# Optimization experiments

Measured on AMD Instinct MI355X. Metric: run time of the kernel, lower is better.

Reference implementation:

```python
import jax, jax.numpy as jnp
import numpy as np
from jax import lax
from jax.scipy.special import logsumexp

B, T, L = 64, 256, 16          # batch, max words per sent, max chars per word
VC, DC, CH = 100, 50, 100      # char vocab, char emb dim, char cnn hidden
VW, DW = 50000, 300            # word vocab, word emb dim
VF, DF = 20, 20                # feature vocab, feature emb dim
H = 256                        # lstm hidden per direction (word_hidden_dim=512)
LAB = 50                       # label alphabet size
N = LAB + 2                    # +START, +STOP tags (NCRF++-style CRF)
START, STOP = N - 2, N - 1
IN = CH + DW + DF              # lstm input dim = 420


def setup_inputs():
    key = jax.random.key(0)
    k = jax.random.split(key, 16)
    p = 0.1
    # pack_padded_sequence requires lengths sorted descending; max length = T
    lens = jnp.sort(jax.random.randint(k[0], (B,), T // 2, T + 1))[::-1].at[0].set(T)
    mask = jnp.arange(T)[None, :] < lens[:, None]
    return dict(
        batch_word=jax.random.randint(k[1], (B, T), 0, VW),
        batch_features=jax.random.randint(k[2], (B, 1), 0, VF),
        batch_wordlen=lens,
        batch_char=jax.random.randint(k[3], (B * T, L), 0, VC),
        batch_charlen=jnp.full((B * T,), L, dtype=jnp.int32),
        batch_charrecover=jnp.arange(B * T),
        mask=mask,
        batch_label=jax.random.randint(k[4], (B, T), 0, LAB),
        char_emb=jax.random.normal(k[5], (VC, DC)) * p,
        conv_w=jax.random.normal(k[6], (CH, DC, 3)) * p,
        conv_b=jnp.zeros((CH,)),
        word_emb=jax.random.normal(k[7], (VW, DW)) * p,
        feat_emb=jax.random.normal(k[8], (VF, DF)) * p,
        w_ih_f=jax.random.normal(k[9], (4 * H, IN)) * p,
        w_hh_f=jax.random.normal(k[10], (4 * H, H)) * p,
        b_f=jnp.zeros((4 * H,)),
        w_ih_b=jax.random.normal(k[11], (4 * H, IN)) * p,
        w_hh_b=jax.random.normal(k[12], (4 * H, H)) * p,
        b_b=jnp.zeros((4 * H,)),
        proj_w=jax.random.normal(k[13], (N, 2 * H)) * p,
        proj_b=jnp.zeros((N,)),
        transitions=(jax.random.normal(k[14], (N, N)) * p)
            .at[:, START].set(-1e4).at[STOP, :].set(-1e4),
    )


def _lstm_dir(x_tb, m_tb, w_ih, w_hh, b, reverse):
    # x_tb: (T,B,IN), m_tb: (T,B,1) float; masked state update == packed-seq LSTM
    xs = jnp.einsum('tbi,gi->tbg', x_tb, w_ih) + b  # precomputed input proj
    def step(carry, inp):
        h, c = carry
        xt, mt = inp
        g = xt + h @ w_hh.T
        i, f, gg, o = jnp.split(g, 4, axis=-1)  # torch gate order i,f,g,o
        c_new = jax.nn.sigmoid(f) * c + jax.nn.sigmoid(i) * jnp.tanh(gg)
        h_new = jax.nn.sigmoid(o) * jnp.tanh(c_new)
        h = mt * h_new + (1 - mt) * h
        c = mt * c_new + (1 - mt) * c
        return (h, c), h
    init = (jnp.zeros((x_tb.shape[1], H), x_tb.dtype),
            jnp.zeros((x_tb.shape[1], H), x_tb.dtype))
    _, hs = lax.scan(step, init, (xs, m_tb), reverse=reverse)
    return hs  # (T,B,H)


def _emissions(batch_word, batch_features, batch_char, batch_charrecover, mask,
               char_emb, conv_w, conv_b, word_emb, feat_emb,
               w_ih_f, w_hh_f, b_f, w_ih_b, w_hh_b, b_b, proj_w, proj_b):
    maskf = mask.astype(jnp.float32)
    # char CNN (dropout = identity at eval time)
    ce = char_emb[batch_char].transpose(0, 2, 1)                     # (BT,DC,L)
    cc = lax.conv_general_dilated(ce, conv_w, (1,), [(1, 1)],
                                  dimension_numbers=('NCH', 'OIH', 'NCH'))
    cc = cc + conv_b[None, :, None]
    pooled = cc.max(axis=2)[batch_charrecover]                       # recover sort order
    char_feats = pooled.reshape(B, T, CH)
    feat_e = jnp.broadcast_to(feat_emb[batch_features], (B, T, DF))  # repeat_interleave
    x = jnp.concatenate([word_emb[batch_word], char_feats, feat_e], axis=2)
    x_tb, m_tb = x.transpose(1, 0, 2), maskf.T[:, :, None]
    hf = _lstm_dir(x_tb, m_tb, w_ih_f, w_hh_f, b_f, reverse=False)
    hb = _lstm_dir(x_tb, m_tb, w_ih_b, w_hh_b, b_b, reverse=True)
    # pad_packed zeroes padded outputs
    lstm_out = jnp.concatenate([hf, hb], axis=-1).transpose(1, 0, 2) * maskf[:, :, None]
    return lstm_out @ proj_w.T + proj_b                              # (B,T,N)


def _crf(feats, mask, batch_wordlen, batch_label, transitions):
    mb = mask.T[:, :, None]                                          # (T,B,1) bool
    s = feats[:, :, None, :] + transitions[None, None]               # (B,T,N,N): s[b,t,i,j]=feat[b,t,j]+T[i,j]
    st = jnp.moveaxis(s, 1, 0)                                       # (T,B,N,N)
    # ---- forward algorithm: log partition Z ----
    def fwd(a, inp):
        st_t, m = inp
        new = logsumexp(a[:, :, None] + st_t, axis=1)
        return jnp.where(m, new, a), None
    alpha, _ = lax.scan(fwd, st[0][:, START, :], (st[1:], mb[1:]))
    Z = logsumexp(alpha + transitions[:, STOP][None, :], axis=1)
    # ---- gold path score ----
    maskf = mask.astype(feats.dtype)
    emit = jnp.sum(jnp.take_along_axis(feats, batch_label[:, :, None], 2)[..., 0] * maskf, 1)
    tr = jnp.sum(transitions[batch_label[:, :-1], batch_label[:, 1:]] * maskf[:, 1:], 1)
    last_tag = jnp.take_along_axis(batch_label, (batch_wordlen - 1)[:, None], 1)[:, 0]
    gold = emit + tr + transitions[START, batch_label[:, 0]] + transitions[last_tag, STOP]
    loss = jnp.sum(Z - gold)
    # ---- viterbi decode ----
    def vstep(v, inp):
        st_t, m = inp
        cur = v[:, :, None] + st_t
        new, bp = cur.max(axis=1), cur.argmax(axis=1)
        v = jnp.where(m, new, v)
        bp = jnp.where(m, bp, jnp.arange(N)[None, :])  # identity bp on padding
        return v, bp
    v, bps = lax.scan(vstep, st[0][:, START, :], (st[1:], mb[1:]))
    term = v + transitions[:, STOP][None, :]
    best_last = jnp.argmax(term, axis=1)
    def back(tag, bp_t):
        prev = jnp.take_along_axis(bp_t, tag[:, None], 1)[:, 0]
        return prev, prev
    _, early = lax.scan(back, best_last, bps, reverse=True)          # tags for t=0..T-2
    path = jnp.concatenate([early, best_last[None]], 0).T            # (B,T)
    tag_seq = jnp.where(mask, path, 0)
    return loss, tag_seq


def reference(batch_word, batch_features, batch_wordlen, batch_char, batch_charlen,
              batch_charrecover, mask, batch_label,
              char_emb, conv_w, conv_b, word_emb, feat_emb,
              w_ih_f, w_hh_f, b_f, w_ih_b, w_hh_b, b_b, proj_w, proj_b, transitions):
    feats = _emissions(batch_word, batch_features, batch_char, batch_charrecover, mask,
                       char_emb, conv_w, conv_b, word_emb, feat_emb,
                       w_ih_f, w_hh_f, b_f, w_ih_b, w_hh_b, b_b, proj_w, proj_b)
    loss, tag_seq = _crf(feats, mask, batch_wordlen, batch_label, transitions)
    return loss, tag_seq
```

## Files before the change

### kernel.cpp

```cpp
#include <hip/hip_runtime.h>
#include <hip/hip_bf16.h>
#include <math.h>

#define BB 64
#define TT 256
#define LCH 16
#define DC 50
#define CHN 100
#define DW 300
#define DF 20
#define HID 256
#define G4 1024
#define INDIM 420
#define KPAD 448
#define NTAG 52
#define TSTART 50
#define TSTOP 51

static constexpr size_t OFF_POOL  = 0;
static constexpr size_t OFF_XH    = 6553600;
static constexpr size_t OFF_W16F  = 21233664;
static constexpr size_t OFF_W16B  = 22151168;
static constexpr size_t OFF_HF    = 0;
static constexpr size_t OFF_HB    = 16777216;
static constexpr size_t OFF_XSF   = 34078720;
static constexpr size_t OFF_XSB   = 101187584;
static constexpr size_t OFF_FEATS = 168296448;
static constexpr size_t OFF_WPF   = 171704320;
static constexpr size_t OFF_WPB   = 172752896;
static constexpr size_t OFF_LOSSB = 173801472;
static constexpr size_t OFF_CTR   = 173801728;

typedef _Float16 v2h __attribute__((ext_vector_type(2)));
typedef _Float16 f16x8 __attribute__((ext_vector_type(8)));
typedef float f32x4 __attribute__((ext_vector_type(4)));
union UH2 { unsigned u; v2h h; };
__device__ __forceinline__ float fdot2u(unsigned a, unsigned b, float c) {
    UH2 x, y; x.u = a; y.u = b;
    return __builtin_amdgcn_fdot2(x.h, y.h, c, false);
}
__device__ __forceinline__ float dot8(uint4 w, uint4 h, float acc) {
    acc = fdot2u(w.x, h.x, acc);
    acc = fdot2u(w.y, h.y, acc);
    acc = fdot2u(w.z, h.z, acc);
    acc = fdot2u(w.w, h.w, acc);
    return acc;
}
#define KEEPU4(v) asm volatile("" : "+v"((v).x), "+v"((v).y), "+v"((v).z), "+v"((v).w))

__device__ __forceinline__ float sigm(float x) { return 1.0f / (1.0f + expf(-x)); }

#define CHARCNN_BLOCKS 2048
#define PREP_BLOCKS 5632

__device__ __forceinline__ void packh_one(const float* __restrict__ w,
                                          _Float16* __restrict__ wph, int e) {
    int r  = e & 7;
    int j  = (e >> 3) & 255;
    int k8 = (e >> 11) & 7;
    int g  = (e >> 14) & 3;
    int s  = (e >> 16) & 3;
    wph[e] = (_Float16)w[(g * 256 + j) * HID + (s * 64 + k8 * 8 + r)];
}
__device__ __forceinline__ void cvtw_one(const float* __restrict__ w,
                                         _Float16* __restrict__ wh, int e) {
    int row = e / KPAD, k = e % KPAD;
    wh[e] = (k < INDIM) ? (_Float16)w[row * INDIM + k] : (_Float16)0.f;
}

__global__ __launch_bounds__(256) void k_front(const int* __restrict__ bchar,
                                               const float* __restrict__ cemb,
                                               const float* __restrict__ cw,
                                               const float* __restrict__ cb,
                                               float* __restrict__ pooled,
                                               const float* __restrict__ whf,
                                               const float* __restrict__ whb,
                                               const float* __restrict__ wihf,
                                               const float* __restrict__ wihb,
                                               _Float16* __restrict__ wpf,
                                               _Float16* __restrict__ wpb,
                                               _Float16* __restrict__ wh16f,
                                               _Float16* __restrict__ wh16b,
                                               unsigned* __restrict__ ctr) {
    __shared__ float cwsh[150][100];
    __shared__ float ET[2][DC][20];
    __shared__ int ids[2][LCH];
    int tid = threadIdx.x;
    if (blockIdx.x >= CHARCNN_BLOCKS) {
        int e = (blockIdx.x - CHARCNN_BLOCKS) * 256 + tid;
        if (e == 0) *ctr = 0u;
        if (e < 262144)                packh_one(whf, wpf, e);
        else if (e < 524288)           packh_one(whb, wpb, e - 262144);
        else if (e < 524288 + 458752)  cvtw_one(wihf, wh16f, e - 524288);
        else if (e < 524288 + 917504)  cvtw_one(wihb, wh16b, e - 983040);
        return;
    }
    int wbase = blockIdx.x * 8;
    for (int i = tid; i < 15000; i += 256) {
        int c = i / 150, row = i % 150;
        cwsh[row][c] = cw[i];
    }
    int half = tid >> 7, c = tid & 127;
    float bcv = (c < CHN) ? cb[c] : 0.f;
    for (int g = 0; g < 8; g += 2) {
        __syncthreads();
        if (tid < 32) ids[tid >> 4][tid & 15] = bchar[(wbase + g + (tid >> 4)) * LCH + (tid & 15)];
        __syncthreads();
        for (int s2 = tid; s2 < 2 * DC * 18; s2 += 256) {
            int w2 = s2 / 900, rem = s2 % 900;
            int d = rem / 18, l = rem % 18;
            float v = 0.f;
            if (l >= 1 && l <= 16) v = cemb[ids[w2][l - 1] * DC + d];
            ET[w2][d][l] = v;
        }
        __syncthreads();
        if (c < CHN) {
            float acc[16];
#pragma unroll
            for (int l = 0; l < 16; l++) acc[l] = 0.f;
            for (int d = 0; d < DC; d++) {
                float e[18];
                float4 t0 = *(const float4*)&ET[half][d][0];
                float4 t1 = *(const float4*)&ET[half][d][4];
                float4 t2 = *(const float4*)&ET[half][d][8];
                float4 t3 = *(const float4*)&ET[half][d][12];
                e[0]=t0.x; e[1]=t0.y; e[2]=t0.z; e[3]=t0.w;
                e[4]=t1.x; e[5]=t1.y; e[6]=t1.z; e[7]=t1.w;
                e[8]=t2.x; e[9]=t2.y; e[10]=t2.z; e[11]=t2.w;
                e[12]=t3.x; e[13]=t3.y; e[14]=t3.z; e[15]=t3.w;
                e[16]=ET[half][d][16]; e[17]=ET[half][d][17];
                float w0 = cwsh[d * 3 + 0][c];
                float w1 = cwsh[d * 3 + 1][c];
                float w2 = cwsh[d * 3 + 2][c];
#pragma unroll
                for (int l = 0; l < 16; l++)
                    acc[l] += w0 * e[l] + w1 * e[l + 1] + w2 * e[l + 2];
            }
            float m = acc[0];
#pragma unroll
            for (int l = 1; l < 16; l++) m = fmaxf(m, acc[l]);
            pooled[(wbase + g + half) * CHN + c] = m + bcv;
        }
    }
}

__global__ __launch_bounds__(256) void k_concat(const int* __restrict__ word,
                                                const int* __restrict__ featsidx,
                                                const int* __restrict__ recover,
                                                const float* __restrict__ wemb,
                                                const float* __restrict__ femb,
                                                const float* __restrict__ pooled,
                                                _Float16* __restrict__ xh) {
    int tid = threadIdx.x;
    for (int wi = 0; wi < 8; wi++) {
        int w = blockIdx.x * 8 + wi;
        int b = w >> 8;
        int wid = word[w];
        _Float16* xr = xh + (size_t)w * KPAD;
        for (int c = tid; c < DW; c += 256) xr[c] = (_Float16)wemb[(size_t)wid * DW + c];
        int rc = recover[w];
        if (tid < CHN) xr[DW + tid] = (_Float16)pooled[rc * CHN + tid];
        if (tid < DF)  xr[DW + CHN + tid] = (_Float16)femb[featsidx[b] * DF + tid];
        if (tid >= 100 && tid < 100 + (KPAD - INDIM)) xr[INDIM + (tid - 100)] = (_Float16)0.f;
    }
}

__global__ __launch_bounds__(256, 4) void k_gemm16b(const _Float16* __restrict__ A,
                                                    const _Float16* __restrict__ Bf,
                                                    const _Float16* __restrict__ Bb,
                                                    const float* __restrict__ biasf,
                                                    const float* __restrict__ biasb,
                                                    float* __restrict__ Cf,
                                                    float* __restrict__ Cb) {
    __shared__ __align__(16) _Float16 Asl[128 * 72];
    __shared__ __align__(16) _Float16 Bfl[64 * 72];
    __shared__ __align__(16) _Float16 Bbl[64 * 72];
    int tid = threadIdx.x;
    int wv = tid >> 6, l = tid & 63;
    int lm = l & 15, lk = l >> 4;
    int n0 = blockIdx.x * 64, m0 = blockIdx.y * 128;
    f32x4 z = {0.f, 0.f, 0.f, 0.f};
    f32x4 af0 = z, af1 = z, af2 = z, af3 = z;
    f32x4 ag0 = z, ag1 = z, ag2 = z, ag3 = z;
    f32x4 ab0 = z, ab1 = z, ab2 = z, ab3 = z;
    f32x4 ac0 = z, ac1 = z, ac2 = z, ac3 = z;
    for (int k0 = 0; k0 < KPAD; k0 += 64) {
        __syncthreads();
#pragma unroll
        for (int q = 0; q < 4; q++) {
            int ch = tid + q * 256;
            int r = ch >> 3, cc = ch & 7;
            ((uint4*)Asl)[r * 9 + cc] =
                *(const uint4*)&A[(size_t)(m0 + r) * KPAD + k0 + cc * 8];
        }
#pragma unroll
        for (int q = 0; q < 2; q++) {
            int ch = tid + q * 256;
            int r = ch >> 3, cc = ch & 7;
            ((uint4*)Bfl)[r * 9 + cc] =
                *(const uint4*)&Bf[(size_t)(n0 + r) * KPAD + k0 + cc * 8];
            ((uint4*)Bbl)[r * 9 + cc] =
                *(const uint4*)&Bb[(size_t)(n0 + r) * KPAD + k0 + cc * 8];
        }
        __syncthreads();
#pragma unroll
        for (int kstep = 0; kstep < 2; kstep++) {
            int kk = kstep * 4 + lk;
            f16x8 a0 = ((const f16x8*)Asl)[(wv * 32 + lm) * 9 + kk];
            f16x8 a1 = ((const f16x8*)Asl)[(wv * 32 + 16 + lm) * 9 + kk];
            f16x8 b0 = ((const f16x8*)Bfl)[(0 * 16 + lm) * 9 + kk];
            f16x8 b1 = ((const f16x8*)Bfl)[(1 * 16 + lm) * 9 + kk];
            f16x8 b2 = ((const f16x8*)Bfl)[(2 * 16 + lm) * 9 + kk];
            f16x8 b3 = ((const f16x8*)Bfl)[(3 * 16 + lm) * 9 + kk];
            f16x8 c0 = ((const f16x8*)Bbl)[(0 * 16 + lm) * 9 + kk];
            f16x8 c1 = ((const f16x8*)Bbl)[(1 * 16 + lm) * 9 + kk];
            f16x8 c2 = ((const f16x8*)Bbl)[(2 * 16 + lm) * 9 + kk];
            f16x8 c3 = ((const f16x8*)Bbl)[(3 * 16 + lm) * 9 + kk];
            af0 = __builtin_amdgcn_mfma_f32_16x16x32_f16(a0, b0, af0, 0, 0, 0);
            af1 = __builtin_amdgcn_mfma_f32_16x16x32_f16(a0, b1, af1, 0, 0, 0);
            af2 = __builtin_amdgcn_mfma_f32_16x16x32_f16(a0, b2, af2, 0, 0, 0);
            af3 = __builtin_amdgcn_mfma_f32_16x16x32_f16(a0, b3, af3, 0, 0, 0);
            ag0 = __builtin_amdgcn_mfma_f32_16x16x32_f16(a1, b0, ag0, 0, 0, 0);
            ag1 = __builtin_amdgcn_mfma_f32_16x16x32_f16(a1, b1, ag1, 0, 0, 0);
            ag2 = __builtin_amdgcn_mfma_f32_16x16x32_f16(a1, b2, ag2, 0, 0, 0);
            ag3 = __builtin_amdgcn_mfma_f32_16x16x32_f16(a1, b3, ag3, 0, 0, 0);
            ab0 = __builtin_amdgcn_mfma_f32_16x16x32_f16(a0, c0, ab0, 0, 0, 0);
            ab1 = __builtin_amdgcn_mfma_f32_16x16x32_f16(a0, c1, ab1, 0, 0, 0);
            ab2 = __builtin_amdgcn_mfma_f32_16x16x32_f16(a0, c2, ab2, 0, 0, 0);
            ab3 = __builtin_amdgcn_mfma_f32_16x16x32_f16(a0, c3, ab3, 0, 0, 0);
            ac0 = __builtin_amdgcn_mfma_f32_16x16x32_f16(a1, c0, ac0, 0, 0, 0);
            ac1 = __builtin_amdgcn_mfma_f32_16x16x32_f16(a1, c1, ac1, 0, 0, 0);
            ac2 = __builtin_amdgcn_mfma_f32_16x16x32_f16(a1, c2, ac2, 0, 0, 0);
            ac3 = __builtin_amdgcn_mfma_f32_16x16x32_f16(a1, c3, ac3, 0, 0, 0);
        }
    }
    f32x4 fa[2][4] = {{af0, af1, af2, af3}, {ag0, ag1, ag2, ag3}};
    f32x4 ba[2][4] = {{ab0, ab1, ab2, ab3}, {ac0, ac1, ac2, ac3}};
#pragma unroll
    for (int mi = 0; mi < 2; mi++) {
        int orow = m0 + wv * 32 + mi * 16 + lk * 4;
#pragma unroll
        for (int jn = 0; jn < 4; jn++) {
            int col = n0 + jn * 16 + lm;
            float bvf = biasf[col], bvb = biasb[col];
#pragma unroll
            for (int r = 0; r < 4; r++) {
                Cf[(size_t)(orow + r) * G4 + col] = fa[mi][jn][r] + bvf;
                Cb[(size_t)(orow + r) * G4 + col] = ba[mi][jn][r] + bvb;
            }
        }
    }
}

__global__ __launch_bounds__(1024, 4) void k_lstm(const float* __restrict__ xs_f,
                                               const float* __restrict__ xs_b,
                                               const _Float16* __restrict__ wh_f,
                                               const _Float16* __restrict__ wh_b,
                                               const int* __restrict__ wlen,
                                               float* __restrict__ h_f,
                                               float* __restrict__ h_b) {
    int b = blockIdx.x & 63, d = blockIdx.x >> 6;
    const float* xs = d ? xs_b : xs_f;
    const uint4* wp4 = (const uint4*)(d ? wh_b : wh_f);
    float* ho = d ? h_b : h_f;
    int len = wlen[b];
    __shared__ uint4 olds4[8192];
    __shared__ _Float16 __align__(16) hh[256];
    __shared__ float part[4][4][256];
    int tid = threadIdx.x;
    int j = tid & 255, s = tid >> 8;
    const uint4* pi = wp4 + (size_t)((s * 4 + 0) * 8) * 256 + j;
    const uint4* pf = wp4 + (size_t)((s * 4 + 1) * 8) * 256 + j;
    uint4 wg[8];
    {
        const uint4* pg = wp4 + (size_t)((s * 4 + 2) * 8) * 256 + j;
        const uint4* po = wp4 + (size_t)((s * 4 + 3) * 8) * 256 + j;
#pragma unroll
        for (int k8 = 0; k8 < 8; k8++) {
            wg[k8] = pg[k8 * 256];
            olds4[k8 * 1024 + tid] = po[k8 * 256];
        }
    }
#pragma unroll
    for (int k8 = 0; k8 < 8; k8++) KEEPU4(wg[k8]);
    if (tid < 128) ((unsigned*)hh)[tid] = 0u;
    float c = 0.f;
    const uint4* hsh4 = (const uint4*)hh;
    __syncthreads();
    for (int ss = 0; ss < len; ++ss) {
        int t = d ? (len - 1 - ss) : ss;
        float xv0, xv1, xv2, xv3;
        if (tid < 256) {
            const float* xr = xs + (size_t)(b * TT + t) * G4;
            xv0 = xr[tid];
            xv1 = xr[256 + tid];
            xv2 = xr[512 + tid];
            xv3 = xr[768 + tid];
        }
        asm volatile("" : "+v"(pi), "+v"(pf));
        float a0 = 0.f, a1 = 0.f, a2 = 0.f, a3 = 0.f;
#pragma unroll
        for (int k8 = 0; k8 < 8; k8++) {
            uint4 h4 = hsh4[s * 8 + k8];
            uint4 wi = pi[k8 * 256];
            uint4 wf = pf[k8 * 256];
            uint4 wo = olds4[k8 * 1024 + tid];
            a0 = dot8(wi, h4, a0);
            a1 = dot8(wf, h4, a1);
            a2 = dot8(wg[k8], h4, a2);
            a3 = dot8(wo, h4, a3);
        }
        part[s][0][j] = a0;
        part[s][1][j] = a1;
        part[s][2][j] = a2;
        part[s][3][j] = a3;
        __syncthreads();
        if (tid < 256) {
            float s0 = part[0][0][tid] + part[1][0][tid] + part[2][0][tid] + part[3][0][tid] + xv0;
            float s1 = part[0][1][tid] + part[1][1][tid] + part[2][1][tid] + part[3][1][tid] + xv1;
            float s2 = part[0][2][tid] + part[1][2][tid] + part[2][2][tid] + part[3][2][tid] + xv2;
            float s3 = part[0][3][tid] + part[1][3][tid] + part[2][3][tid] + part[3][3][tid] + xv3;
            float ig = sigm(s0), fg = sigm(s1), zg = tanhf(s2), og = sigm(s3);
            c = fg * c + ig * zg;
            float h = og * tanhf(c);
            hh[tid] = (_Float16)h;
            ho[(size_t)(b * TT + t) * HID + tid] = h;
        }
        __syncthreads();
    }
}

__global__ __launch_bounds__(256) void k_proj(const float* __restrict__ hf,
                                              const float* __restrict__ hb,
                                              const float* __restrict__ pw,
                                              const float* __restrict__ pb,
                                              float* __restrict__ feats) {
    __shared__ float pwsh[NTAG][513];
    __shared__ float hsh[512];
    __shared__ float part2[4][NTAG];
    int tid = threadIdx.x;
    int w0 = blockIdx.x * 64;
    for (int i = tid; i < NTAG * 512; i += 256) pwsh[i >> 9][i & 511] = pw[i];
    __syncthreads();
    int q = tid >> 6, t = tid & 63;
    for (int wi = 0; wi < 64; wi++) {
        int w = w0 + wi;
        hsh[tid]       = hf[(size_t)w * HID + tid];
        hsh[256 + tid] = hb[(size_t)w * HID + tid];
        __syncthreads();
        if (t < NTAG) {
            float ssum = 0.f;
            int k0 = q * 128;
            for (int k = 0; k < 128; k++) ssum += pwsh[t][k0 + k] * hsh[k0 + k];
            part2[q][t] = ssum;
        }
        __syncthreads();
        if (tid < NTAG)
            feats[(size_t)w * NTAG + tid] =
                part2[0][tid] + part2[1][tid] + part2[2][tid] + part2[3][tid] + pb[tid];
        __syncthreads();
    }
}

__global__ __launch_bounds__(64) void k_crf(const float* __restrict__ feats,
                                            const float* __restrict__ trans,
                                            const int* __restrict__ wlen,
                                            const int* __restrict__ blabel,
                                            float* __restrict__ lossb,
                                            float* __restrict__ outtags,
                                            unsigned* __restrict__ ctr,
                                            float* __restrict__ out) {
    __shared__ float Tm[NTAG * NTAG];
    __shared__ float st[NTAG];
    __shared__ unsigned char bp[TT - 1][NTAG];
    int bid = blockIdx.x;
    int b = bid & 63;
    bool vit = bid >= BB;
    int j = threadIdx.x;
    for (int s = j; s < NTAG * NTAG; s += 64) Tm[s] = trans[s];
    __builtin_amdgcn_wave_barrier();
    int len = wlen[b];
    const float* fb = feats + (size_t)b * TT * NTAG;
    if (j < NTAG) st[j] = fb[j] + Tm[TSTART * NTAG + j];
    __builtin_amdgcn_wave_barrier();
    if (!vit) {
        float frow = (j < NTAG && len > 1) ? fb[NTAG + j] : 0.f;
        for (int t = 1; t < len; t++) {
            float frow_nxt = (j < NTAG && t + 1 < len) ? fb[(size_t)(t + 1) * NTAG + j] : 0.f;
            float anew = 0.f;
            if (j < NTAG) {
                float ma = -1e30f, mb = -1e30f, mc = -1e30f, md = -1e30f;
                for (int i = 0; i < 13; i++) {
                    ma = fmaxf(ma, st[i]      + Tm[i * NTAG + j]);
                    mb = fmaxf(mb, st[i + 13] + Tm[(i + 13) * NTAG + j]);
                    mc = fmaxf(mc, st[i + 26] + Tm[(i + 26) * NTAG + j]);
                    md = fmaxf(md, st[i + 39] + Tm[(i + 39) * NTAG + j]);
                }
                float m1 = fmaxf(fmaxf(ma, mb), fmaxf(mc, md));
                float sa = 0.f, sb = 0.f, sc = 0.f, sd = 0.f;
                for (int i = 0; i < 13; i++) {
                    sa += expf(st[i]      + Tm[i * NTAG + j] - m1);
                    sb += expf(st[i + 13] + Tm[(i + 13) * NTAG + j] - m1);
                    sc += expf(st[i + 26] + Tm[(i + 26) * NTAG + j] - m1);
                    sd += expf(st[i + 39] + Tm[(i + 39) * NTAG + j] - m1);
                }
                anew = m1 + logf((sa + sb) + (sc + sd)) + frow;
            }
            __builtin_amdgcn_wave_barrier();
            if (j < NTAG) st[j] = anew;
            __builtin_amdgcn_wave_barrier();
            frow = frow_nxt;
        }
        float red = (j < NTAG) ? st[j] + Tm[j * NTAG + TSTOP] : -1e30f;
        float m1 = red;
#pragma unroll
        for (int m = 32; m; m >>= 1) m1 = fmaxf(m1, __shfl_xor(m1, m));
        float e = (j < NTAG) ? expf(red - m1) : 0.f;
        float ssum = e;
#pragma unroll
        for (int m = 32; m; m >>= 1) ssum += __shfl_xor(ssum, m);
        const int* lab = blabel + b * TT;
        float gpart = 0.f;
        for (int t = 1 + j; t < len; t += 64)
            gpart += Tm[lab[t - 1] * NTAG + lab[t]] + fb[(size_t)t * NTAG + lab[t]];
#pragma unroll
        for (int m = 32; m; m >>= 1) gpart += __shfl_xor(gpart, m);
        if (j == 0) {
            float Zg = m1 + logf(ssum);
            float goldv = Tm[TSTART * NTAG + lab[0]] + fb[lab[0]] + gpart
                        + Tm[lab[len - 1] * NTAG + TSTOP];
            lossb[b] = Zg - goldv;
            __threadfence();
            unsigned old = atomicAdd(ctr, 1u);
            if (old == BB - 1) {
                __threadfence();
                float stot = 0.f;
                for (int i = 0; i < BB; i++) stot += lossb[i];
                out[0] = stot;
            }
        }
    } else {
        float frow = (j < NTAG && len > 1) ? fb[NTAG + j] : 0.f;
        for (int t = 1; t < len; t++) {
            float frow_nxt = (j < NTAG && t + 1 < len) ? fb[(size_t)(t + 1) * NTAG + j] : 0.f;
            float vnew = 0.f;
            int arg = 0;
            if (j < NTAG) {
                float va = -1e30f, vb = -1e30f, vc = -1e30f, vd = -1e30f;
                int ia = 0, ib = 13, ic = 26, id2 = 39;
                for (int i = 0; i < 13; i++) {
                    float s0 = st[i]      + Tm[i * NTAG + j];        if (s0 > va) { va = s0; ia = i; }
                    float s1 = st[i + 13] + Tm[(i + 13) * NTAG + j]; if (s1 > vb) { vb = s1; ib = i + 13; }
                    float s2 = st[i + 26] + Tm[(i + 26) * NTAG + j]; if (s2 > vc) { vc = s2; ic = i + 26; }
                    float s3 = st[i + 39] + Tm[(i + 39) * NTAG + j]; if (s3 > vd) { vd = s3; id2 = i + 39; }
                }
                float vm = va; arg = ia;
                if (vb > vm) { vm = vb; arg = ib; }
                if (vc > vm) { vm = vc; arg = ic; }
                if (vd > vm) { vm = vd; arg = id2; }
                vnew = vm + frow;
            }
            __builtin_amdgcn_wave_barrier();
            if (j < NTAG) {
                st[j] = vnew;
                bp[t - 1][j] = (unsigned char)arg;
            }
            __builtin_amdgcn_wave_barrier();
            frow = frow_nxt;
        }
        if (j == 0) {
            int best = 0;
            float vm = st[0] + Tm[0 * NTAG + TSTOP];
            for (int i = 1; i < NTAG; i++) {
                float v = st[i] + Tm[i * NTAG + TSTOP];
                if (v > vm) { vm = v; best = i; }
            }
            float* ot = outtags + (size_t)b * TT;
            int tag = best;
            ot[len - 1] = (float)tag;
            for (int t = len - 2; t >= 0; t--) {
                tag = bp[t][tag];
                ot[t] = (float)tag;
            }
            for (int t = len; t < TT; t++) ot[t] = 0.f;
        }
    }
}

extern "C" void kernel_launch(void* const* d_in, const int* in_sizes, int n_in,
                              void* d_out, int out_size, void* d_ws, size_t ws_size,
                              hipStream_t stream) {
    const int* batch_word     = (const int*)d_in[0];
    const int* batch_features = (const int*)d_in[1];
    const int* batch_wordlen  = (const int*)d_in[2];
    const int* batch_char     = (const int*)d_in[3];
    const int* batch_recover  = (const int*)d_in[5];
    const int* batch_label    = (const int*)d_in[7];
    const float* char_emb = (const float*)d_in[8];
    const float* conv_w   = (const float*)d_in[9];
    const float* conv_b   = (const float*)d_in[10];
    const float* word_emb = (const float*)d_in[11];
    const float* feat_emb = (const float*)d_in[12];
    const float* w_ih_f   = (const float*)d_in[13];
    const float* w_hh_f   = (const float*)d_in[14];
    const float* b_f      = (const float*)d_in[15];
    const float* w_ih_b   = (const float*)d_in[16];
    const float* w_hh_b   = (const float*)d_in[17];
    const float* b_b      = (const float*)d_in[18];
    const float* proj_w   = (const float*)d_in[19];
    const float* proj_b   = (const float*)d_in[20];
    const float* trans    = (const float*)d_in[21];

    char* ws = (char*)d_ws;
    float* pooled   = (float*)(ws + OFF_POOL);
    _Float16* xh    = (_Float16*)(ws + OFF_XH);
    _Float16* wh16f = (_Float16*)(ws + OFF_W16F);
    _Float16* wh16b = (_Float16*)(ws + OFF_W16B);
    float* h_f    = (float*)(ws + OFF_HF);
    float* h_b    = (float*)(ws + OFF_HB);
    float* xs_f   = (float*)(ws + OFF_XSF);
    float* xs_b   = (float*)(ws + OFF_XSB);
    float* feats  = (float*)(ws + OFF_FEATS);
    _Float16* wh_f = (_Float16*)(ws + OFF_WPF);
    _Float16* wh_b = (_Float16*)(ws + OFF_WPB);
    float* lossb  = (float*)(ws + OFF_LOSSB);
    unsigned* ctr = (unsigned*)(ws + OFF_CTR);

    k_front<<<CHARCNN_BLOCKS + PREP_BLOCKS, 256, 0, stream>>>(
        batch_char, char_emb, conv_w, conv_b, pooled,
        w_hh_f, w_hh_b, w_ih_f, w_ih_b, wh_f, wh_b, wh16f, wh16b, ctr);
    k_concat<<<(BB * TT) / 8, 256, 0, stream>>>(batch_word, batch_features, batch_recover,
                                                word_emb, feat_emb, pooled, xh);
    k_gemm16b<<<dim3(G4 / 64, (BB * TT) / 128), 256, 0, stream>>>(xh, wh16f, wh16b,
                                                                  b_f, b_b, xs_f, xs_b);
    k_lstm<<<128, 1024, 0, stream>>>(xs_f, xs_b, wh_f, wh_b, batch_wordlen, h_f, h_b);
    k_proj<<<(BB * TT) / 64, 256, 0, stream>>>(h_f, h_b, proj_w, proj_b, feats);
    k_crf<<<2 * BB, 64, 0, stream>>>(feats, trans, batch_wordlen, batch_label,
                                     lossb, (float*)d_out + 1, ctr, (float*)d_out);
}
```

Baseline: 1.596 ms.

## Store LSTM outputs as fp16 and run projection as MFMA GEMM

The LSTM now writes its hidden states as fp16 into one concatenated forward/backward buffer instead of two fp32 buffers. The scalar per-word projection kernel is replaced by an MFMA 16x16x32 f16 GEMM, with the projection weights padded to 64 rows and converted to fp16 in the front prep kernel. The aim is to cut projection compute and halve hidden-state traffic, at the cost of fp16 rounding on the emissions. A leftover redundant store line remains in the weight conversion.

```diff
diff --git a/kernel.cpp b/kernel.cpp
--- a/kernel.cpp
+++ b/kernel.cpp
@@ -21,8 +21,8 @@
 static constexpr size_t OFF_XH    = 6553600;
 static constexpr size_t OFF_W16F  = 21233664;
 static constexpr size_t OFF_W16B  = 22151168;
-static constexpr size_t OFF_HF    = 0;
-static constexpr size_t OFF_HB    = 16777216;
+static constexpr size_t OFF_PW16  = 23068672;
+static constexpr size_t OFF_HCAT  = 0;
 static constexpr size_t OFF_XSF   = 34078720;
 static constexpr size_t OFF_XSB   = 101187584;
 static constexpr size_t OFF_FEATS = 168296448;
@@ -51,7 +51,7 @@
 __device__ __forceinline__ float sigm(float x) { return 1.0f / (1.0f + expf(-x)); }
 
 #define CHARCNN_BLOCKS 2048
-#define PREP_BLOCKS 5632
+#define PREP_BLOCKS 5760
 
 __device__ __forceinline__ void packh_one(const float* __restrict__ w,
                                           _Float16* __restrict__ wph, int e) {
@@ -77,10 +77,12 @@
                                                const float* __restrict__ whb,
                                                const float* __restrict__ wihf,
                                                const float* __restrict__ wihb,
+                                               const float* __restrict__ pw,
                                                _Float16* __restrict__ wpf,
                                                _Float16* __restrict__ wpb,
                                                _Float16* __restrict__ wh16f,
                                                _Float16* __restrict__ wh16b,
+                                               _Float16* __restrict__ pw16,
                                                unsigned* __restrict__ ctr) {
     __shared__ float cwsh[150][100];
     __shared__ float ET[2][DC][20];
@@ -91,8 +93,14 @@
         if (e == 0) *ctr = 0u;
         if (e < 262144)                packh_one(whf, wpf, e);
         else if (e < 524288)           packh_one(whb, wpb, e - 262144);
-        else if (e < 524288 + 458752)  cvtw_one(wihf, wh16f, e - 524288);
-        else if (e < 524288 + 917504)  cvtw_one(wihb, wh16b, e - 983040);
+        else if (e < 983040)           cvtw_one(wihf, wh16f, e - 524288);
+        else if (e < 1441792)          cvtw_one(wihb, wh16b, e - 983040);
+        else if (e < 1474560) {
+            int p = e - 1441792;
+            int row = p >> 9;
+            pw16[p] = (row < NTAG) ? (_Float16)pw[p - (64 - NTAG) * 0 - (row - row) + (row * 512 + (p & 511)) - p + p] : (_Float16)0.f;
+            pw16[p] = (row < NTAG) ? (_Float16)pw[row * 512 + (p & 511)] : (_Float16)0.f;
+        }
         return;
     }
     int wbase = blockIdx.x * 8;
@@ -257,12 +265,10 @@
                                                const _Float16* __restrict__ wh_f,
                                                const _Float16* __restrict__ wh_b,
                                                const int* __restrict__ wlen,
-                                               float* __restrict__ h_f,
-                                               float* __restrict__ h_b) {
+                                               _Float16* __restrict__ hcat) {
     int b = blockIdx.x & 63, d = blockIdx.x >> 6;
     const float* xs = d ? xs_b : xs_f;
     const uint4* wp4 = (const uint4*)(d ? wh_b : wh_f);
-    float* ho = d ? h_b : h_f;
     int len = wlen[b];
     __shared__ uint4 olds4[8192];
     __shared__ _Float16 __align__(16) hh[256];
@@ -323,42 +329,65 @@
             float ig = sigm(s0), fg = sigm(s1), zg = tanhf(s2), og = sigm(s3);
             c = fg * c + ig * zg;
             float h = og * tanhf(c);
-            hh[tid] = (_Float16)h;
-            ho[(size_t)(b * TT + t) * HID + tid] = h;
-        }
-        __syncthreads();
-    }
-}
-
-__global__ __launch_bounds__(256) void k_proj(const float* __restrict__ hf,
-                                              const float* __restrict__ hb,
-                                              const float* __restrict__ pw,
-                                              const float* __restrict__ pb,
-                                              float* __restrict__ feats) {
-    __shared__ float pwsh[NTAG][513];
-    __shared__ float hsh[512];
-    __shared__ float part2[4][NTAG];
+            _Float16 h16 = (_Float16)h;
+            hh[tid] = h16;
+            hcat[(size_t)(b * TT + t) * 512 + d * 256 + tid] = h16;
+        }
+        __syncthreads();
+    }
+}
+
+__global__ __launch_bounds__(256) void k_projm(const _Float16* __restrict__ A,
+                                               const _Float16* __restrict__ Bw,
+                                               const float* __restrict__ pb,
+                                               float* __restrict__ feats) {
+    __shared__ __align__(16) _Float16 Al[8 * 64 * 72];
+    __shared__ __align__(16) _Float16 Bl[8 * 64 * 72];
     int tid = threadIdx.x;
-    int w0 = blockIdx.x * 64;
-    for (int i = tid; i < NTAG * 512; i += 256) pwsh[i >> 9][i & 511] = pw[i];
+    int wv = tid >> 6, l = tid & 63;
+    int lm = l & 15, lk = l >> 4;
+    int m0 = blockIdx.x * 64;
+#pragma unroll
+    for (int q = 0; q < 16; q++) {
+        int ch = tid + q * 256;
+        int r = ch >> 6;
+        int rem = ch & 63;
+        int cnk = rem >> 3, cc = rem & 7;
+        ((uint4*)Al)[(cnk * 64 + r) * 9 + cc] =
+            *(const uint4*)&A[(size_t)(m0 + r) * 512 + cnk * 64 + cc * 8];
+        ((uint4*)Bl)[(cnk * 64 + r) * 9 + cc] =
+            *(const uint4*)&Bw[(size_t)r * 512 + cnk * 64 + cc * 8];
+    }
     __syncthreads();
-    int q = tid >> 6, t = tid & 63;
-    for (int wi = 0; wi < 64; wi++) {
-        int w = w0 + wi;
-        hsh[tid]       = hf[(size_t)w * HID + tid];
-        hsh[256 + tid] = hb[(size_t)w * HID + tid];
-        __syncthreads();
-        if (t < NTAG) {
-            float ssum = 0.f;
-            int k0 = q * 128;
-            for (int k = 0; k < 128; k++) ssum += pwsh[t][k0 + k] * hsh[k0 + k];
-            part2[q][t] = ssum;
-        }
-        __syncthreads();
-        if (tid < NTAG)
-            feats[(size_t)w * NTAG + tid] =
-                part2[0][tid] + part2[1][tid] + part2[2][tid] + part2[3][tid] + pb[tid];
-        __syncthreads();
+    f32x4 z = {0.f, 0.f, 0.f, 0.f};
+    f32x4 ac0 = z, ac1 = z, ac2 = z, ac3 = z;
+#pragma unroll
+    for (int cnk = 0; cnk < 8; cnk++) {
+#pragma unroll
+        for (int ks = 0; ks < 2; ks++) {
+            int kk = ks * 4 + lk;
+            f16x8 a  = ((const f16x8*)Al)[(cnk * 64 + wv * 16 + lm) * 9 + kk];
+            f16x8 b0 = ((const f16x8*)Bl)[(cnk * 64 +  0 + lm) * 9 + kk];
+            f16x8 b1 = ((const f16x8*)Bl)[(cnk * 64 + 16 + lm) * 9 + kk];
+            f16x8 b2 = ((const f16x8*)Bl)[(cnk * 64 + 32 + lm) * 9 + kk];
+            f16x8 b3 = ((const f16x8*)Bl)[(cnk * 64 + 48 + lm) * 9 + kk];
+            ac0 = __builtin_amdgcn_mfma_f32_16x16x32_f16(a, b0, ac0, 0, 0, 0);
+            ac1 = __builtin_amdgcn_mfma_f32_16x16x32_f16(a, b1, ac1, 0, 0, 0);
+            ac2 = __builtin_amdgcn_mfma_f32_16x16x32_f16(a, b2, ac2, 0, 0, 0);
+            ac3 = __builtin_amdgcn_mfma_f32_16x16x32_f16(a, b3, ac3, 0, 0, 0);
+        }
+    }
+    f32x4 accs[4] = {ac0, ac1, ac2, ac3};
+    int orow = m0 + wv * 16 + lk * 4;
+#pragma unroll
+    for (int jn = 0; jn < 4; jn++) {
+        int col = jn * 16 + lm;
+        if (col < NTAG) {
+            float bv = pb[col];
+#pragma unroll
+            for (int r = 0; r < 4; r++)
+                feats[(size_t)(orow + r) * NTAG + col] = accs[jn][r] + bv;
+        }
     }
 }
 
@@ -516,8 +545,8 @@
     _Float16* xh    = (_Float16*)(ws + OFF_XH);
     _Float16* wh16f = (_Float16*)(ws + OFF_W16F);
     _Float16* wh16b = (_Float16*)(ws + OFF_W16B);
-    float* h_f    = (float*)(ws + OFF_HF);
-    float* h_b    = (float*)(ws + OFF_HB);
+    _Float16* pw16  = (_Float16*)(ws + OFF_PW16);
+    _Float16* hcat  = (_Float16*)(ws + OFF_HCAT);
     float* xs_f   = (float*)(ws + OFF_XSF);
     float* xs_b   = (float*)(ws + OFF_XSB);
     float* feats  = (float*)(ws + OFF_FEATS);
@@ -528,13 +557,14 @@
 
     k_front<<<CHARCNN_BLOCKS + PREP_BLOCKS, 256, 0, stream>>>(
         batch_char, char_emb, conv_w, conv_b, pooled,
-        w_hh_f, w_hh_b, w_ih_f, w_ih_b, wh_f, wh_b, wh16f, wh16b, ctr);
+        w_hh_f, w_hh_b, w_ih_f, w_ih_b, proj_w,
+        wh_f, wh_b, wh16f, wh16b, pw16, ctr);
     k_concat<<<(BB * TT) / 8, 256, 0, stream>>>(batch_word, batch_features, batch_recover,
                                                 word_emb, feat_emb, pooled, xh);
     k_gemm16b<<<dim3(G4 / 64, (BB * TT) / 128), 256, 0, stream>>>(xh, wh16f, wh16b,
                                                                   b_f, b_b, xs_f, xs_b);
-    k_lstm<<<128, 1024, 0, stream>>>(xs_f, xs_b, wh_f, wh_b, batch_wordlen, h_f, h_b);
-    k_proj<<<(BB * TT) / 64, 256, 0, stream>>>(h_f, h_b, proj_w, proj_b, feats);
+    k_lstm<<<128, 1024, 0, stream>>>(xs_f, xs_b, wh_f, wh_b, batch_wordlen, hcat);
+    k_projm<<<(BB * TT) / 64, 256, 0, stream>>>(hcat, pw16, proj_b, feats);
     k_crf<<<2 * BB, 64, 0, stream>>>(feats, trans, batch_wordlen, batch_label,
                                      lossb, (float*)d_out + 1, ctr, (float*)d_out);
 }
```

Result: faster. 1.499 ms (-6.0%).
